# Optimization experiments

Measured on AMD Instinct MI355X. Metric: run time of the kernel, lower is better.

Reference implementation:

```python
import jax, jax.numpy as jnp
import numpy as np

DT = 0.05
TAU = 0.15
SIGMA = float(np.sqrt(2.0 * DT / TAU))  # GaussianNoise default sigma
NOISE_SCALE = 1.0

N = 2048        # nneurons
RANK = 64       # nbg
BATCH = 2048
IN_DIM = 128    # input_sources['stim'] size


def setup_inputs() -> dict:
    key = jax.random.key(0)
    ks = jax.random.split(key, 10)
    inv_sqrt_n = 1.0 / np.sqrt(N)
    return {
        "r_thalamic": jax.random.uniform(ks[0], (BATCH, RANK), jnp.float32),
        "stim": jax.random.normal(ks[1], (BATCH, IN_DIM), jnp.float32),
        "x": jax.random.normal(ks[2], (BATCH, N), jnp.float32) * inv_sqrt_n,
        "r": jax.nn.softplus(jax.random.normal(ks[3], (BATCH, N), jnp.float32) * inv_sqrt_n),
        "J": jax.random.normal(ks[4], (N, N), jnp.float32) * (1.2 * inv_sqrt_n),
        "B": jax.random.normal(ks[5], (1, N), jnp.float32),
        "U": jax.random.normal(ks[6], (N, RANK), jnp.float32) * inv_sqrt_n,
        "V": jax.random.normal(ks[7], (RANK, N), jnp.float32) * inv_sqrt_n,
        "I_stim": jax.random.normal(ks[8], (IN_DIM, N), jnp.float32) * inv_sqrt_n,
        "eps": jax.random.normal(ks[9], (BATCH, N), jnp.float32),
    }


def reference(r_thalamic, stim, x, r, J, B, U, V, I_stim, eps):
    # external input: stim @ I['stim']  -> (batch, N)
    ext = stim @ I_stim
    # bg_tensor @ r == U @ diag(r_thalamic) @ V @ r, computed in low-rank form:
    # (batch, rank) * (batch, rank) -> project back with U
    rec_input = (r_thalamic * (r @ V.T)) @ U.T          # (batch, N)
    pre = -x + r @ J + rec_input + B + ext               # (batch, N)
    noisy = pre + (SIGMA * NOISE_SCALE) * eps            # GaussianNoise
    x_new = x + (DT / TAU) * noisy
    r_new = jax.nn.softplus(x_new)
    return (x_new, r_new)
```

## Files before the change

kernel.cpp:

```cpp
#include <hip/hip_runtime.h>
#include <cstdint>
#include <cstddef>


#define K_TOT 2240
#define NN    2048

using frag_ab = __attribute__((ext_vector_type(8))) short;
using frag_cd = __attribute__((ext_vector_type(4))) float;

__device__ __forceinline__ unsigned short f2bf(float f) {
  union { float f; unsigned int i; } v;
  v.f = f;
  unsigned int r = v.i + 0x7fffu + ((v.i >> 16) & 1u);
  return (unsigned short)(r >> 16);
}

__device__ __forceinline__ uint4 cvt8(const float* __restrict__ p) {
  float4 a = *(const float4*)p;
  float4 b = *(const float4*)(p + 4);
  union { uint4 v; unsigned short u[8]; } d;
  d.u[0] = f2bf(a.x); d.u[1] = f2bf(a.y); d.u[2] = f2bf(a.z); d.u[3] = f2bf(a.w);
  d.u[4] = f2bf(b.x); d.u[5] = f2bf(b.y); d.u[6] = f2bf(b.z); d.u[7] = f2bf(b.w);
  return d.v;
}

__device__ __forceinline__ void gl_lds16(const void* g, void* l) {
  __builtin_amdgcn_global_load_lds(
      (const __attribute__((address_space(1))) void*)g,
      (__attribute__((address_space(3))) void*)l, 16, 0, 0);
}

__global__ __launch_bounds__(256) void prep(
    const float* __restrict__ J, const float* __restrict__ Ist,
    const float* __restrict__ rg, const float* __restrict__ stim,
    const float* __restrict__ U, unsigned short* __restrict__ Ap,
    unsigned short* __restrict__ Bp) {
  __shared__ unsigned short tile[64 * 66];
  const int blk = blockIdx.x;
  const int t = threadIdx.x;
  if (blk < 1088) {
    const float* src;
    int srcC = 2048, dst_off, cx, cy;
    if (blk < 1024) { src = J;   dst_off = 0;    cx = blk & 31; cy = blk >> 5; }
    else            { src = Ist; dst_off = 2048; cx = (blk - 1024) & 31; cy = (blk - 1024) >> 5; }
    const int r0 = cy * 64, c0 = cx * 64;
    const int sr = t >> 3, c8 = t & 7;
#pragma unroll
    for (int p = 0; p < 2; ++p) {
      const int row = sr + 32 * p;
      union { uint4 v; unsigned short u[8]; } d;
      d.v = cvt8(&src[(size_t)(r0 + row) * srcC + c0 + c8 * 8]);
#pragma unroll
      for (int e = 0; e < 8; ++e) tile[row * 66 + c8 * 8 + e] = d.u[e];
    }
    __syncthreads();
#pragma unroll
    for (int p = 0; p < 2; ++p) {
      const int scol = sr + 32 * p;
      union { uint4 v; unsigned short u[8]; } d;
#pragma unroll
      for (int e = 0; e < 8; ++e) d.u[e] = tile[(c8 * 8 + e) * 66 + scol];
      *(uint4*)&Bp[(size_t)(c0 + scol) * K_TOT + dst_off + r0 + c8 * 8] = d.v;
    }
  } else {
    const int row = blk - 1088;
    *(uint4*)&Ap[(size_t)row * K_TOT + t * 8] = cvt8(&rg[(size_t)row * 2048 + t * 8]);
    if (t < 24) {
      const int c = 256 + t;
      if (c < 272)
        *(uint4*)&Ap[(size_t)row * K_TOT + c * 8] =
            cvt8(&stim[(size_t)row * 128 + (c - 256) * 8]);
      else
        *(uint4*)&Bp[(size_t)row * K_TOT + c * 8] =
            cvt8(&U[(size_t)row * 64 + (c - 272) * 8]);
    }
  }
}

__global__ __launch_bounds__(256) void t_part(
    const float* __restrict__ rg, const float* __restrict__ V,
    float* __restrict__ part) {
  __shared__ alignas(16) unsigned short Ats[32 * 64];
  __shared__ alignas(16) unsigned short Bts[64 * 64];
  const int t = threadIdx.x;
  const int wave = t >> 6, lane = t & 63;
  const int q = lane >> 4, l15 = lane & 15;
  const int mt = blockIdx.x & 63, s = blockIdx.x >> 6;
  const int b0 = mt * 32;
  const int arow = t >> 3, ac8 = t & 7;

  const float* gA  = rg + (size_t)(b0 + arow) * 2048 + s * 512 + ac8 * 8;
  const float* gB0 = V  + (size_t)arow        * 2048 + s * 512 + ac8 * 8;
  const float* gB1 = V  + (size_t)(arow + 32) * 2048 + s * 512 + ac8 * 8;

  frag_cd acc0 = {0.f, 0.f, 0.f, 0.f};
  frag_cd acc1 = {0.f, 0.f, 0.f, 0.f};

  for (int kt = 0; kt < 8; ++kt) {
    const int k0 = kt * 64;
    uint4 va  = cvt8(gA + k0);
    uint4 vb0 = cvt8(gB0 + k0);
    uint4 vb1 = cvt8(gB1 + k0);
    __syncthreads();
    *(uint4*)&Ats[t * 8]        = va;
    *(uint4*)&Bts[t * 8]        = vb0;
    *(uint4*)&Bts[2048 + t * 8] = vb1;
    __syncthreads();
#pragma unroll
    for (int ks = 0; ks < 2; ++ks) {
      frag_ab a0 = *(const frag_ab*)&Ats[(l15)      * 64 + ks * 32 + q * 8];
      frag_ab a1 = *(const frag_ab*)&Ats[(16 + l15) * 64 + ks * 32 + q * 8];
      frag_ab b  = *(const frag_ab*)&Bts[(wave * 16 + l15) * 64 + ks * 32 + q * 8];
      acc0 = __builtin_amdgcn_mfma_f32_16x16x32_bf16(a0, b, acc0, 0, 0, 0);
      acc1 = __builtin_amdgcn_mfma_f32_16x16x32_bf16(a1, b, acc1, 0, 0, 0);
    }
  }
  const int p = wave * 16 + l15;
#pragma unroll
  for (int reg = 0; reg < 4; ++reg) {
    const int m0 = q * 4 + reg;
    part[((size_t)s * 2048 + b0 + m0) * 64 + p]      = acc0[reg];
    part[((size_t)s * 2048 + b0 + m0 + 16) * 64 + p] = acc1[reg];
  }
}

__global__ __launch_bounds__(256) void t_reduce(
    const float* __restrict__ part, const float* __restrict__ tha,
    unsigned short* __restrict__ Ap) {
  const int e = blockIdx.x * 256 + threadIdx.x;
  float4 s0 = *(const float4*)(part + (size_t)e * 4);
  float4 s1 = *(const float4*)(part + 131072 + (size_t)e * 4);
  float4 s2 = *(const float4*)(part + 262144 + (size_t)e * 4);
  float4 s3 = *(const float4*)(part + 393216 + (size_t)e * 4);
  float4 th = *(const float4*)(tha + (size_t)e * 4);
  union { uint2 v; unsigned short u[4]; } o;
  o.u[0] = f2bf(th.x * (s0.x + s1.x + s2.x + s3.x));
  o.u[1] = f2bf(th.y * (s0.y + s1.y + s2.y + s3.y));
  o.u[2] = f2bf(th.z * (s0.z + s1.z + s2.z + s3.z));
  o.u[3] = f2bf(th.w * (s0.w + s1.w + s2.w + s3.w));
  const int b = e >> 4, p0 = (e * 4) & 63;
  *(uint2*)&Ap[(size_t)b * K_TOT + 2176 + p0] = o.v;
}

__global__ __launch_bounds__(256, 2) void main_gemm(
    const unsigned short* __restrict__ Ap, const unsigned short* __restrict__ Bp,
    const float* __restrict__ xg, const float* __restrict__ epsg,
    const float* __restrict__ Bvec,
    float* __restrict__ outx, float* __restrict__ outr) {
  __shared__ alignas(16) unsigned short As[64 * 64];
  __shared__ alignas(16) unsigned short Bs[128 * 64];

  const int t = threadIdx.x;
  const int wave = t >> 6, lane = t & 63;
  const int q = lane >> 4, l15 = lane & 15, l7 = lane & 7;
  const int wm = (wave & 1) * 32, wn = (wave >> 1) * 64;
  const int bm0 = blockIdx.y * 64, bn0 = blockIdx.x * 128;

  const unsigned short* gA[2];
  unsigned short* lA[2];
  const unsigned short* gB[4];
  unsigned short* lB[4];
#pragma unroll
  for (int r = 0; r < 2; ++r) {
    const int ci = r * 256 + t;
    const int row = ci >> 3;
    const int lc = (ci & 7) ^ (row & 7);
    gA[r] = Ap + (size_t)(bm0 + row) * K_TOT + lc * 8;
    lA[r] = As + (size_t)(r * 256 + wave * 64) * 8;
  }
#pragma unroll
  for (int r = 0; r < 4; ++r) {
    const int ci = r * 256 + t;
    const int row = ci >> 3;
    const int lc = (ci & 7) ^ (row & 7);
    gB[r] = Bp + (size_t)(bn0 + row) * K_TOT + lc * 8;
    lB[r] = Bs + (size_t)(r * 256 + wave * 64) * 8;
  }

  frag_cd acc[2][4];
#pragma unroll
  for (int i = 0; i < 2; ++i)
#pragma unroll
    for (int j = 0; j < 4; ++j) {
      frag_cd z = {0.f, 0.f, 0.f, 0.f};
      acc[i][j] = z;
    }

  for (int kt = 0; kt < 35; ++kt) {
    const int k0 = kt * 64;
    __syncthreads();
#pragma unroll
    for (int r = 0; r < 2; ++r) gl_lds16(gA[r] + k0, lA[r]);
#pragma unroll
    for (int r = 0; r < 4; ++r) gl_lds16(gB[r] + k0, lB[r]);
    __syncthreads();
#pragma unroll
    for (int ks = 0; ks < 2; ++ks) {
      const int lc = ks * 4 + q;
      frag_ab af[2], bfr[4];
#pragma unroll
      for (int i = 0; i < 2; ++i) {
        const int ra = wm + i * 16 + l15;
        af[i] = *(const frag_ab*)&As[ra * 64 + ((lc ^ l7) * 8)];
      }
#pragma unroll
      for (int j = 0; j < 4; ++j) {
        const int rb = wn + j * 16 + l15;
        bfr[j] = *(const frag_ab*)&Bs[rb * 64 + ((lc ^ l7) * 8)];
      }
#pragma unroll
      for (int i = 0; i < 2; ++i)
#pragma unroll
        for (int j = 0; j < 4; ++j)
          acc[i][j] = __builtin_amdgcn_mfma_f32_16x16x32_bf16(af[i], bfr[j], acc[i][j], 0, 0, 0);
    }
  }

  const float A_DT = 0.33333334f;
  const float SIG  = 0.81649658092772615f;
#pragma unroll
  for (int j = 0; j < 4; ++j) {
    const int nc = bn0 + wn + j * 16 + l15;
    const float bvf = Bvec[nc];
#pragma unroll
    for (int i = 0; i < 2; ++i) {
#pragma unroll
      for (int reg = 0; reg < 4; ++reg) {
        const int mr = bm0 + wm + i * 16 + q * 4 + reg;
        const size_t off = (size_t)mr * NN + nc;
        const float xf = xg[off];
        const float ef = epsg[off];
        const float xn = xf + A_DT * (acc[i][j][reg] + bvf - xf + SIG * ef);
        outx[off] = xn;
        outr[off] = (xn > 20.f) ? xn : log1pf(__expf(xn));
      }
    }
  }
}

extern "C" void kernel_launch(void* const* d_in, const int* in_sizes, int n_in,
                              void* d_out, int out_size, void* d_ws, size_t ws_size,
                              hipStream_t stream) {
  (void)in_sizes; (void)n_in; (void)out_size; (void)ws_size;
  const float* tha  = (const float*)d_in[0];
  const float* stim = (const float*)d_in[1];
  const float* x    = (const float*)d_in[2];
  const float* r    = (const float*)d_in[3];
  const float* J    = (const float*)d_in[4];
  const float* Bv   = (const float*)d_in[5];
  const float* U    = (const float*)d_in[6];
  const float* V    = (const float*)d_in[7];
  const float* Ist  = (const float*)d_in[8];
  const float* eps  = (const float*)d_in[9];

  unsigned short* Apk = (unsigned short*)d_ws;
  unsigned short* Bpk = Apk + (size_t)NN * K_TOT;
  float* outx = (float*)d_out;
  float* outr = outx + (size_t)NN * NN;
  float* tpart = (float*)d_out;

  prep<<<3136, 256, 0, stream>>>(J, Ist, r, stim, U, Apk, Bpk);
  t_part<<<256, 256, 0, stream>>>(r, V, tpart);
  t_reduce<<<128, 256, 0, stream>>>(tpart, tha, Apk);
  main_gemm<<<dim3(16, 32), 256, 0, stream>>>(Apk, Bpk, x, eps, Bv, outx, outr);
}
```

Baseline: 186.2 us.

## Fuse low-rank projection into prep and reduction into GEMM, shrink GEMM tile

```diff
diff --git a/kernel.cpp b/kernel.cpp
--- a/kernel.cpp
+++ b/kernel.cpp
@@ -3,8 +3,9 @@
 #include <cstddef>
 
 
-#define K_TOT 2240
-#define NN    2048
+#define KA 2176
+#define KB 2240
+#define NN 2048
 
 using frag_ab = __attribute__((ext_vector_type(8))) short;
 using frag_cd = __attribute__((ext_vector_type(4))) float;
@@ -34,14 +35,18 @@
 __global__ __launch_bounds__(256) void prep(
     const float* __restrict__ J, const float* __restrict__ Ist,
     const float* __restrict__ rg, const float* __restrict__ stim,
-    const float* __restrict__ U, unsigned short* __restrict__ Ap,
-    unsigned short* __restrict__ Bp) {
+    const float* __restrict__ U, const float* __restrict__ V,
+    unsigned short* __restrict__ Ap, unsigned short* __restrict__ Bp,
+    float* __restrict__ part) {
   __shared__ unsigned short tile[64 * 66];
+  __shared__ alignas(16) unsigned short Ats[32 * 64];
+  __shared__ alignas(16) unsigned short Bts[64 * 64];
   const int blk = blockIdx.x;
   const int t = threadIdx.x;
+
   if (blk < 1088) {
     const float* src;
-    int srcC = 2048, dst_off, cx, cy;
+    int dst_off, cx, cy;
     if (blk < 1024) { src = J;   dst_off = 0;    cx = blk & 31; cy = blk >> 5; }
     else            { src = Ist; dst_off = 2048; cx = (blk - 1024) & 31; cy = (blk - 1024) >> 5; }
     const int r0 = cy * 64, c0 = cx * 64;
@@ -50,7 +55,7 @@
     for (int p = 0; p < 2; ++p) {
       const int row = sr + 32 * p;
       union { uint4 v; unsigned short u[8]; } d;
-      d.v = cvt8(&src[(size_t)(r0 + row) * srcC + c0 + c8 * 8]);
+      d.v = cvt8(&src[(size_t)(r0 + row) * 2048 + c0 + c8 * 8]);
 #pragma unroll
       for (int e = 0; e < 8; ++e) tile[row * 66 + c8 * 8 + e] = d.u[e];
     }
@@ -61,158 +66,173 @@
       union { uint4 v; unsigned short u[8]; } d;
 #pragma unroll
       for (int e = 0; e < 8; ++e) d.u[e] = tile[(c8 * 8 + e) * 66 + scol];
-      *(uint4*)&Bp[(size_t)(c0 + scol) * K_TOT + dst_off + r0 + c8 * 8] = d.v;
-    }
-  } else {
+      *(uint4*)&Bp[(size_t)(c0 + scol) * KB + dst_off + r0 + c8 * 8] = d.v;
+    }
+  } else if (blk < 3136) {
     const int row = blk - 1088;
-    *(uint4*)&Ap[(size_t)row * K_TOT + t * 8] = cvt8(&rg[(size_t)row * 2048 + t * 8]);
+    *(uint4*)&Ap[(size_t)row * KA + t * 8] = cvt8(&rg[(size_t)row * 2048 + t * 8]);
     if (t < 24) {
       const int c = 256 + t;
       if (c < 272)
-        *(uint4*)&Ap[(size_t)row * K_TOT + c * 8] =
+        *(uint4*)&Ap[(size_t)row * KA + c * 8] =
             cvt8(&stim[(size_t)row * 128 + (c - 256) * 8]);
       else
-        *(uint4*)&Bp[(size_t)row * K_TOT + c * 8] =
+        *(uint4*)&Bp[(size_t)row * KB + c * 8] =
             cvt8(&U[(size_t)row * 64 + (c - 272) * 8]);
     }
-  }
-}
-
-__global__ __launch_bounds__(256) void t_part(
-    const float* __restrict__ rg, const float* __restrict__ V,
-    float* __restrict__ part) {
-  __shared__ alignas(16) unsigned short Ats[32 * 64];
-  __shared__ alignas(16) unsigned short Bts[64 * 64];
-  const int t = threadIdx.x;
-  const int wave = t >> 6, lane = t & 63;
-  const int q = lane >> 4, l15 = lane & 15;
-  const int mt = blockIdx.x & 63, s = blockIdx.x >> 6;
-  const int b0 = mt * 32;
-  const int arow = t >> 3, ac8 = t & 7;
-
-  const float* gA  = rg + (size_t)(b0 + arow) * 2048 + s * 512 + ac8 * 8;
-  const float* gB0 = V  + (size_t)arow        * 2048 + s * 512 + ac8 * 8;
-  const float* gB1 = V  + (size_t)(arow + 32) * 2048 + s * 512 + ac8 * 8;
-
-  frag_cd acc0 = {0.f, 0.f, 0.f, 0.f};
-  frag_cd acc1 = {0.f, 0.f, 0.f, 0.f};
-
-  for (int kt = 0; kt < 8; ++kt) {
-    const int k0 = kt * 64;
-    uint4 va  = cvt8(gA + k0);
-    uint4 vb0 = cvt8(gB0 + k0);
-    uint4 vb1 = cvt8(gB1 + k0);
-    __syncthreads();
-    *(uint4*)&Ats[t * 8]        = va;
-    *(uint4*)&Bts[t * 8]        = vb0;
-    *(uint4*)&Bts[2048 + t * 8] = vb1;
-    __syncthreads();
-#pragma unroll
-    for (int ks = 0; ks < 2; ++ks) {
-      frag_ab a0 = *(const frag_ab*)&Ats[(l15)      * 64 + ks * 32 + q * 8];
-      frag_ab a1 = *(const frag_ab*)&Ats[(16 + l15) * 64 + ks * 32 + q * 8];
-      frag_ab b  = *(const frag_ab*)&Bts[(wave * 16 + l15) * 64 + ks * 32 + q * 8];
-      acc0 = __builtin_amdgcn_mfma_f32_16x16x32_bf16(a0, b, acc0, 0, 0, 0);
-      acc1 = __builtin_amdgcn_mfma_f32_16x16x32_bf16(a1, b, acc1, 0, 0, 0);
-    }
-  }
-  const int p = wave * 16 + l15;
-#pragma unroll
-  for (int reg = 0; reg < 4; ++reg) {
-    const int m0 = q * 4 + reg;
-    part[((size_t)s * 2048 + b0 + m0) * 64 + p]      = acc0[reg];
-    part[((size_t)s * 2048 + b0 + m0 + 16) * 64 + p] = acc1[reg];
-  }
-}
-
-__global__ __launch_bounds__(256) void t_reduce(
+  } else {
+    const int tb = blk - 3136;
+    const int mt = tb & 63, s = tb >> 6;
+    const int b0 = mt * 32;
+    const int wave = t >> 6, lane = t & 63;
+    const int q = lane >> 4, l15 = lane & 15;
+    const int arow = t >> 3, ac8 = t & 7;
+
+    const float* gA  = rg + (size_t)(b0 + arow) * 2048 + s * 512 + ac8 * 8;
+    const float* gB0 = V  + (size_t)arow        * 2048 + s * 512 + ac8 * 8;
+    const float* gB1 = V  + (size_t)(arow + 32) * 2048 + s * 512 + ac8 * 8;
+
+    frag_cd acc0 = {0.f, 0.f, 0.f, 0.f};
+    frag_cd acc1 = {0.f, 0.f, 0.f, 0.f};
+
+    for (int kt = 0; kt < 8; ++kt) {
+      const int k0 = kt * 64;
+      uint4 va  = cvt8(gA + k0);
+      uint4 vb0 = cvt8(gB0 + k0);
+      uint4 vb1 = cvt8(gB1 + k0);
+      __syncthreads();
+      *(uint4*)&Ats[t * 8]        = va;
+      *(uint4*)&Bts[t * 8]        = vb0;
+      *(uint4*)&Bts[2048 + t * 8] = vb1;
+      __syncthreads();
+#pragma unroll
+      for (int ks = 0; ks < 2; ++ks) {
+        frag_ab a0 = *(const frag_ab*)&Ats[(l15)      * 64 + ks * 32 + q * 8];
+        frag_ab a1 = *(const frag_ab*)&Ats[(16 + l15) * 64 + ks * 32 + q * 8];
+        frag_ab b  = *(const frag_ab*)&Bts[(wave * 16 + l15) * 64 + ks * 32 + q * 8];
+        acc0 = __builtin_amdgcn_mfma_f32_16x16x32_bf16(a0, b, acc0, 0, 0, 0);
+        acc1 = __builtin_amdgcn_mfma_f32_16x16x32_bf16(a1, b, acc1, 0, 0, 0);
+      }
+    }
+    const int p = wave * 16 + l15;
+#pragma unroll
+    for (int reg = 0; reg < 4; ++reg) {
+      const int m0 = q * 4 + reg;
+      part[((size_t)s * 2048 + b0 + m0) * 64 + p]      = acc0[reg];
+      part[((size_t)s * 2048 + b0 + m0 + 16) * 64 + p] = acc1[reg];
+    }
+  }
+}
+
+__global__ __launch_bounds__(256, 4) void main_gemm(
+    const unsigned short* __restrict__ Ap, const unsigned short* __restrict__ Bp,
     const float* __restrict__ part, const float* __restrict__ tha,
-    unsigned short* __restrict__ Ap) {
-  const int e = blockIdx.x * 256 + threadIdx.x;
-  float4 s0 = *(const float4*)(part + (size_t)e * 4);
-  float4 s1 = *(const float4*)(part + 131072 + (size_t)e * 4);
-  float4 s2 = *(const float4*)(part + 262144 + (size_t)e * 4);
-  float4 s3 = *(const float4*)(part + 393216 + (size_t)e * 4);
-  float4 th = *(const float4*)(tha + (size_t)e * 4);
-  union { uint2 v; unsigned short u[4]; } o;
-  o.u[0] = f2bf(th.x * (s0.x + s1.x + s2.x + s3.x));
-  o.u[1] = f2bf(th.y * (s0.y + s1.y + s2.y + s3.y));
-  o.u[2] = f2bf(th.z * (s0.z + s1.z + s2.z + s3.z));
-  o.u[3] = f2bf(th.w * (s0.w + s1.w + s2.w + s3.w));
-  const int b = e >> 4, p0 = (e * 4) & 63;
-  *(uint2*)&Ap[(size_t)b * K_TOT + 2176 + p0] = o.v;
-}
-
-__global__ __launch_bounds__(256, 2) void main_gemm(
-    const unsigned short* __restrict__ Ap, const unsigned short* __restrict__ Bp,
     const float* __restrict__ xg, const float* __restrict__ epsg,
     const float* __restrict__ Bvec,
     float* __restrict__ outx, float* __restrict__ outr) {
   __shared__ alignas(16) unsigned short As[64 * 64];
-  __shared__ alignas(16) unsigned short Bs[128 * 64];
+  __shared__ alignas(16) unsigned short Bs[64 * 64];
 
   const int t = threadIdx.x;
   const int wave = t >> 6, lane = t & 63;
   const int q = lane >> 4, l15 = lane & 15, l7 = lane & 7;
-  const int wm = (wave & 1) * 32, wn = (wave >> 1) * 64;
-  const int bm0 = blockIdx.y * 64, bn0 = blockIdx.x * 128;
+  const int wm = (wave & 1) * 32, wn = (wave >> 1) * 32;
+  const int bm0 = blockIdx.y * 64, bn0 = blockIdx.x * 64;
 
   const unsigned short* gA[2];
+  const unsigned short* gB[2];
   unsigned short* lA[2];
-  const unsigned short* gB[4];
-  unsigned short* lB[4];
+  unsigned short* lB[2];
+  uint4 tval[2];
 #pragma unroll
   for (int r = 0; r < 2; ++r) {
     const int ci = r * 256 + t;
     const int row = ci >> 3;
     const int lc = (ci & 7) ^ (row & 7);
-    gA[r] = Ap + (size_t)(bm0 + row) * K_TOT + lc * 8;
+    gA[r] = Ap + (size_t)(bm0 + row) * KA + lc * 8;
+    gB[r] = Bp + (size_t)(bn0 + row) * KB + lc * 8;
     lA[r] = As + (size_t)(r * 256 + wave * 64) * 8;
-  }
-#pragma unroll
-  for (int r = 0; r < 4; ++r) {
-    const int ci = r * 256 + t;
-    const int row = ci >> 3;
-    const int lc = (ci & 7) ^ (row & 7);
-    gB[r] = Bp + (size_t)(bn0 + row) * K_TOT + lc * 8;
     lB[r] = Bs + (size_t)(r * 256 + wave * 64) * 8;
-  }
-
-  frag_cd acc[2][4];
+
+    const int p0 = lc * 8;
+    const size_t base = ((size_t)(bm0 + row)) * 64 + p0;
+    float4 s0 = *(const float4*)&part[base];
+    float4 s1 = *(const float4*)&part[base + 4];
+#pragma unroll
+    for (int s = 1; s < 4; ++s) {
+      float4 a = *(const float4*)&part[(size_t)s * 131072 + base];
+      float4 b = *(const float4*)&part[(size_t)s * 131072 + base + 4];
+      s0.x += a.x; s0.y += a.y; s0.z += a.z; s0.w += a.w;
+      s1.x += b.x; s1.y += b.y; s1.z += b.z; s1.w += b.w;
+    }
+    float4 th0 = *(const float4*)&tha[base];
+    float4 th1 = *(const float4*)&tha[base + 4];
+    union { uint4 v; unsigned short u[8]; } d;
+    d.u[0] = f2bf(th0.x * s0.x); d.u[1] = f2bf(th0.y * s0.y);
+    d.u[2] = f2bf(th0.z * s0.z); d.u[3] = f2bf(th0.w * s0.w);
+    d.u[4] = f2bf(th1.x * s1.x); d.u[5] = f2bf(th1.y * s1.y);
+    d.u[6] = f2bf(th1.z * s1.z); d.u[7] = f2bf(th1.w * s1.w);
+    tval[r] = d.v;
+  }
+
+  frag_cd acc[2][2];
 #pragma unroll
   for (int i = 0; i < 2; ++i)
 #pragma unroll
-    for (int j = 0; j < 4; ++j) {
+    for (int j = 0; j < 2; ++j) {
       frag_cd z = {0.f, 0.f, 0.f, 0.f};
       acc[i][j] = z;
     }
 
-  for (int kt = 0; kt < 35; ++kt) {
+#pragma unroll 1
+  for (int kt = 0; kt < 34; ++kt) {
     const int k0 = kt * 64;
     __syncthreads();
 #pragma unroll
-    for (int r = 0; r < 2; ++r) gl_lds16(gA[r] + k0, lA[r]);
-#pragma unroll
-    for (int r = 0; r < 4; ++r) gl_lds16(gB[r] + k0, lB[r]);
+    for (int r = 0; r < 2; ++r) {
+      gl_lds16(gA[r] + k0, lA[r]);
+      gl_lds16(gB[r] + k0, lB[r]);
+    }
     __syncthreads();
 #pragma unroll
     for (int ks = 0; ks < 2; ++ks) {
       const int lc = ks * 4 + q;
-      frag_ab af[2], bfr[4];
+      frag_ab af[2], bfr[2];
 #pragma unroll
       for (int i = 0; i < 2; ++i) {
-        const int ra = wm + i * 16 + l15;
-        af[i] = *(const frag_ab*)&As[ra * 64 + ((lc ^ l7) * 8)];
-      }
-#pragma unroll
-      for (int j = 0; j < 4; ++j) {
-        const int rb = wn + j * 16 + l15;
-        bfr[j] = *(const frag_ab*)&Bs[rb * 64 + ((lc ^ l7) * 8)];
+        af[i]  = *(const frag_ab*)&As[(wm + i * 16 + l15) * 64 + ((lc ^ l7) * 8)];
+        bfr[i] = *(const frag_ab*)&Bs[(wn + i * 16 + l15) * 64 + ((lc ^ l7) * 8)];
       }
 #pragma unroll
       for (int i = 0; i < 2; ++i)
 #pragma unroll
-        for (int j = 0; j < 4; ++j)
+        for (int j = 0; j < 2; ++j)
+          acc[i][j] = __builtin_amdgcn_mfma_f32_16x16x32_bf16(af[i], bfr[j], acc[i][j], 0, 0, 0);
+    }
+  }
+
+  {
+    const int k0 = 34 * 64;
+    __syncthreads();
+#pragma unroll
+    for (int r = 0; r < 2; ++r) {
+      *(uint4*)&As[(size_t)(r * 256 + t) * 8] = tval[r];
+      gl_lds16(gB[r] + k0, lB[r]);
+    }
+    __syncthreads();
+#pragma unroll
+    for (int ks = 0; ks < 2; ++ks) {
+      const int lc = ks * 4 + q;
+      frag_ab af[2], bfr[2];
+#pragma unroll
+      for (int i = 0; i < 2; ++i) {
+        af[i]  = *(const frag_ab*)&As[(wm + i * 16 + l15) * 64 + ((lc ^ l7) * 8)];
+        bfr[i] = *(const frag_ab*)&Bs[(wn + i * 16 + l15) * 64 + ((lc ^ l7) * 8)];
+      }
+#pragma unroll
+      for (int i = 0; i < 2; ++i)
+#pragma unroll
+        for (int j = 0; j < 2; ++j)
           acc[i][j] = __builtin_amdgcn_mfma_f32_16x16x32_bf16(af[i], bfr[j], acc[i][j], 0, 0, 0);
     }
   }
@@ -220,7 +240,7 @@
   const float A_DT = 0.33333334f;
   const float SIG  = 0.81649658092772615f;
 #pragma unroll
-  for (int j = 0; j < 4; ++j) {
+  for (int j = 0; j < 2; ++j) {
     const int nc = bn0 + wn + j * 16 + l15;
     const float bvf = Bvec[nc];
 #pragma unroll
@@ -255,13 +275,12 @@
   const float* eps  = (const float*)d_in[9];
 
   unsigned short* Apk = (unsigned short*)d_ws;
-  unsigned short* Bpk = Apk + (size_t)NN * K_TOT;
+  unsigned short* Bpk = Apk + (size_t)NN * KA;
+  float* part = (float*)(Bpk + (size_t)NN * KB);
   float* outx = (float*)d_out;
   float* outr = outx + (size_t)NN * NN;
-  float* tpart = (float*)d_out;
-
-  prep<<<3136, 256, 0, stream>>>(J, Ist, r, stim, U, Apk, Bpk);
-  t_part<<<256, 256, 0, stream>>>(r, V, tpart);
-  t_reduce<<<128, 256, 0, stream>>>(tpart, tha, Apk);
-  main_gemm<<<dim3(16, 32), 256, 0, stream>>>(Apk, Bpk, x, eps, Bv, outx, outr);
-}
+
+  prep<<<3392, 256, 0, stream>>>(J, Ist, r, stim, U, V, Apk, Bpk, part);
+  main_gemm<<<dim3(32, 32), 256, 0, stream>>>(Apk, Bpk, part, tha, x, eps, Bv,
+                                              outx, outr);
+}
```

After: 181.1 us. -2.7%, faster.
